# Kernel tuning notes

Measured on AMD Instinct MI355X. Metric: run time of the kernel, lower is better.

## Reference

```python
import jax, jax.numpy as jnp
import numpy as np

N, E = 50000, 800000
IN_C, H_C, OUT_C, HEADS = 64, 32, 32, 8


def setup_inputs() -> dict:
    key = jax.random.key(0)
    ks = jax.random.split(key, 16)
    def glorot(k, shape):
        fan_in = shape[-1]
        return jax.random.normal(k, shape, dtype=jnp.float32) / jnp.sqrt(jnp.float32(fan_in))
    inp = {
        'x': jax.random.normal(ks[0], (N, IN_C), dtype=jnp.float32),
        'edge_index': jax.random.randint(ks[1], (2, E), 0, N, dtype=jnp.int64),
        # layer 1: in_c -> h_c, heads
        'W1l': glorot(ks[2], (HEADS * H_C, IN_C)),
        'b1l': jnp.zeros((HEADS * H_C,), jnp.float32),
        'W1r': glorot(ks[3], (HEADS * H_C, IN_C)),
        'b1r': jnp.zeros((HEADS * H_C,), jnp.float32),
        'att1': glorot(ks[4], (HEADS, H_C)),
        'bias1': jnp.zeros((H_C,), jnp.float32),
        # layer 2: h_c -> out_c, heads
        'W2l': glorot(ks[5], (HEADS * OUT_C, H_C)),
        'b2l': jnp.zeros((HEADS * OUT_C,), jnp.float32),
        'W2r': glorot(ks[6], (HEADS * OUT_C, H_C)),
        'b2r': jnp.zeros((HEADS * OUT_C,), jnp.float32),
        'att2': glorot(ks[7], (HEADS, OUT_C)),
        'bias2': jnp.zeros((OUT_C,), jnp.float32),
    }
    return inp


def _gatv2_layer(x, src, dst, valid, Wl, bl, Wr, br, att, bias):
    # PyG GATv2Conv (share_weights=False, concat=False): message j->i uses
    # e = att . leaky_relu(lin_l(x_j) + lin_r(x_i), 0.2); softmax over dst; agg lin_l(x_j).
    n = x.shape[0]
    heads, c = att.shape
    xl = (x @ Wl.T + bl).reshape(n, heads, c)
    xr = (x @ Wr.T + br).reshape(n, heads, c)
    m = jax.nn.leaky_relu(xl[src] + xr[dst], negative_slope=0.2)  # [Etot,H,C]
    score = jnp.einsum('ehc,hc->eh', m, att)                      # [Etot,H]
    score = jnp.where(valid[:, None], score, -jnp.inf)
    smax = jax.ops.segment_max(score, dst, num_segments=n)        # [N,H]
    a = jnp.where(valid[:, None], jnp.exp(score - smax[dst]), 0.0)
    denom = jax.ops.segment_sum(a, dst, num_segments=n)
    a = a / jnp.maximum(denom[dst], 1e-16)
    out = jax.ops.segment_sum(a[..., None] * xl[src], dst, num_segments=n)  # [N,H,C]
    return out.mean(axis=1) + bias


def reference(x, edge_index, W1l, b1l, W1r, b1r, att1, bias1,
              W2l, b2l, W2r, b2r, att2, bias2):
    n = x.shape[0]
    src0, dst0 = edge_index[0], edge_index[1]
    # PyG removes existing self loops then adds fresh ones: mask originals,
    # append one self loop per node (keeps static shapes).
    loop = jnp.arange(n, dtype=src0.dtype)
    src = jnp.concatenate([src0, loop])
    dst = jnp.concatenate([dst0, loop])
    valid = jnp.concatenate([src0 != dst0, jnp.ones((n,), bool)])
    h = _gatv2_layer(x, src, dst, valid, W1l, b1l, W1r, b1r, att1, bias1)
    h = jax.nn.leaky_relu(h, negative_slope=0.01)  # nn.LeakyReLU default
    out = _gatv2_layer(h, src, dst, valid, W2l, b2l, W2r, b2r, att2, bias2)
    return out
```

## Files before the change

### kernel.cpp

```cpp
#include <hip/hip_runtime.h>
#include <math.h>

#define HEADS 8
#define CDIM 32
#define ODIM 256

typedef _Float16 h2 __attribute__((ext_vector_type(2)));
typedef _Float16 h4 __attribute__((ext_vector_type(4)));
typedef _Float16 h8 __attribute__((ext_vector_type(8)));
typedef float f32x4 __attribute__((ext_vector_type(4)));
union H4 { h4 v; h2 p[2]; };

#if __has_builtin(__builtin_amdgcn_fdot2)
#define FDOT2(a,b,c) __builtin_amdgcn_fdot2((a),(b),(c),false)
#else
static __device__ __forceinline__ float fdot2_sw(h2 a, h2 b, float c){
  return fmaf((float)a.x, (float)b.x, fmaf((float)a.y, (float)b.y, c));
}
#define FDOT2(a,b,c) fdot2_sw((a),(b),(c))
#endif

__device__ __forceinline__ float lrelu(float v, float s){ return fmaxf(v, s*v); }

__global__ void block_sum_kernel(const int* __restrict__ counts, int* __restrict__ bsums, int n){
  int i = blockIdx.x*256 + threadIdx.x;
  int v = (i < n) ? counts[i] : 0;
#pragma unroll
  for (int off=1; off<64; off<<=1) v += __shfl_xor(v, off);
  __shared__ int ws[4];
  int lane = threadIdx.x & 63, w = threadIdx.x >> 6;
  if (lane == 0) ws[w] = v;
  __syncthreads();
  if (threadIdx.x == 0) bsums[blockIdx.x] = ws[0]+ws[1]+ws[2]+ws[3];
}

__global__ __launch_bounds__(1024) void scan_bsums_kernel(int* __restrict__ bsums, int nb){
  __shared__ int s[1024];
  int t = threadIdx.x;
  int v = (t < nb) ? bsums[t] : 0;
  s[t] = v;
  __syncthreads();
  for (int off=1; off<1024; off<<=1){
    int u = (t >= off) ? s[t-off] : 0;
    __syncthreads();
    s[t] += u;
    __syncthreads();
  }
  if (t < nb) bsums[t] = s[t] - v;
}

__global__ void local_scan_kernel(const int* __restrict__ counts, const int* __restrict__ bsums,
                                  int* __restrict__ indptr, int n){
  __shared__ int s[256];
  int t = threadIdx.x;
  int i = blockIdx.x*256 + t;
  int v = (i < n) ? counts[i] : 0;
  s[t] = v;
  __syncthreads();
  for (int off=1; off<256; off<<=1){
    int u = (t >= off) ? s[t-off] : 0;
    __syncthreads();
    s[t] += u;
    __syncthreads();
  }
  int excl = s[t] - v + bsums[blockIdx.x];
  if (i < n) indptr[i] = excl;
  if (i == n-1) indptr[n] = excl + v;
}

__global__ void scatter_kernel(const int* __restrict__ src, const int* __restrict__ dst,
                               const int* __restrict__ rank, const int* __restrict__ indptr,
                               int* __restrict__ csr_src, int e){
  int i = blockIdx.x*256 + threadIdx.x;
  if (i < e){
    int r = rank[i];
    if (r >= 0){
      int d = dst[i];
      csr_src[indptr[d] + r] = src[i];
    }
  }
}

template<int K, bool FUSE_COUNT>
__global__ __launch_bounds__(256, 2) void gemm_mfma(const float* __restrict__ X,
    const float* __restrict__ Wl, const float* __restrict__ bl,
    const float* __restrict__ Wr, const float* __restrict__ br,
    _Float16* __restrict__ outl, _Float16* __restrict__ outr, int n,
    const int* __restrict__ src, const int* __restrict__ dst,
    int* __restrict__ counts, int* __restrict__ rank, int e){
  if (FUSE_COUNT && blockIdx.y == 0){
    int stride = gridDim.x*256;
    for (int i = blockIdx.x*256 + threadIdx.x; i < e; i += stride){
      int s = src[i], d = dst[i];
      int r = -1;
      if (s != d) r = atomicAdd(counts + d, 1);
      rank[i] = r;
    }
    return;
  }
  const int KP = K + 8;
  __shared__ __align__(16) _Float16 Xs[64*(K+8)];
  int t = threadIdx.x;
  int n0 = blockIdx.x*64;
  int ybase = FUSE_COUNT ? (blockIdx.y-1) : blockIdx.y;

  for (int idx = t; idx < 64*(K/4); idx += 256){
    int row = idx/(K/4), c = (idx%(K/4))*4;
    int node = n0 + row; if (node >= n) node = n-1;
    float4 xv = *(const float4*)(X + (size_t)node*K + c);
    h4 hv = {(_Float16)xv.x, (_Float16)xv.y, (_Float16)xv.z, (_Float16)xv.w};
    *(h4*)(Xs + row*KP + c) = hv;
  }
  __syncthreads();

  int wave = t >> 6, lane = t & 63;
  int co = ybase*256 + wave*64;
  const float* W   = (co < 256) ? Wl : Wr;
  const float* Bv  = (co < 256) ? bl : br;
  _Float16* outp   = (co < 256) ? outl : outr;
  int lco = co & 255;
  int lr = lane & 15, lg = lane >> 4;

  f32x4 acc[4][4];
#pragma unroll
  for (int c = 0; c < 4; ++c)
#pragma unroll
    for (int m = 0; m < 4; ++m) acc[c][m] = (f32x4){0.f, 0.f, 0.f, 0.f};

#pragma unroll
  for (int ks = 0; ks < K/32; ++ks){
    int k0 = ks*32 + lg*8;
    h8 a[4], b[4];
#pragma unroll
    for (int c = 0; c < 4; ++c){
      const float* wp = W + (size_t)(lco + c*16 + lr)*K + k0;
      float4 w0 = *(const float4*)(wp);
      float4 w1 = *(const float4*)(wp + 4);
      a[c] = (h8){(_Float16)w0.x,(_Float16)w0.y,(_Float16)w0.z,(_Float16)w0.w,
                  (_Float16)w1.x,(_Float16)w1.y,(_Float16)w1.z,(_Float16)w1.w};
    }
#pragma unroll
    for (int m = 0; m < 4; ++m)
      b[m] = *(const h8*)(Xs + (m*16 + lr)*KP + k0);
#pragma unroll
    for (int c = 0; c < 4; ++c)
#pragma unroll
      for (int m = 0; m < 4; ++m)
        acc[c][m] = __builtin_amdgcn_mfma_f32_16x16x32_f16(a[c], b[m], acc[c][m], 0, 0, 0);
  }

#pragma unroll
  for (int c = 0; c < 4; ++c){
    int ch = lco + c*16 + lg*4;
    float4 bb = *(const float4*)(Bv + ch);
#pragma unroll
    for (int m = 0; m < 4; ++m){
      int node = n0 + m*16 + lr;
      if (node < n){
        h4 o = {(_Float16)(acc[c][m][0] + bb.x), (_Float16)(acc[c][m][1] + bb.y),
                (_Float16)(acc[c][m][2] + bb.z), (_Float16)(acc[c][m][3] + bb.w)};
        *(h4*)(outp + (size_t)node*ODIM + ch) = o;
      }
    }
  }
}

__global__ __launch_bounds__(256) void edge_kernel(
    const _Float16* __restrict__ xl, const _Float16* __restrict__ xr,
    const float* __restrict__ att, const float* __restrict__ bias,
    const int* __restrict__ indptr, const int* __restrict__ csr_src,
    float* __restrict__ out, int n, int act)
{
  int wid = blockIdx.x*4 + (threadIdx.x >> 6);
  if (wid >= n) return;
  int lane = threadIdx.x & 63;
  const float LOG2E = 1.44269504088896341f;

  float4 attf = *(const float4*)(att + 4*lane);
  h2 at0 = (h2){(_Float16)(attf.x*LOG2E), (_Float16)(attf.y*LOG2E)};
  h2 at1 = (h2){(_Float16)(attf.z*LOG2E), (_Float16)(attf.w*LOG2E)};
  const h2 c02 = {(_Float16)0.2f, (_Float16)0.2f};

  H4 xrh; xrh.v = *(const h4*)(xr + (size_t)wid*ODIM + 4*lane);
  H4 self; self.v = *(const h4*)(xl + (size_t)wid*ODIM + 4*lane);

  auto score = [&](const H4& c)->float{
    h2 t0 = c.p[0] + xrh.p[0];
    h2 t1 = c.p[1] + xrh.p[1];
    h2 q0 = __builtin_elementwise_max(t0, t0 * c02);
    h2 q1 = __builtin_elementwise_max(t1, t1 * c02);
    float d = FDOT2(q0, at0, FDOT2(q1, at1, 0.f));
    d += __shfl_xor(d, 1);
    d += __shfl_xor(d, 2);
    d += __shfl_xor(d, 4);
    return d;
  };

  float w0 = exp2f(score(self));
  float denom = w0;
  float4 acc;
  acc.x = w0 * (float)self.v.x;
  acc.y = w0 * (float)self.v.y;
  acc.z = w0 * (float)self.v.z;
  acc.w = w0 * (float)self.v.w;

  int beg = __builtin_amdgcn_readfirstlane(indptr[wid]);
  int end = __builtin_amdgcn_readfirstlane(indptr[wid+1]);
  int cnt = end - beg;
  H4 r0, r1;
  r0.v = (h4){}; r1.v = (h4){};
  if (cnt > 0){
    int s0 = __builtin_amdgcn_readfirstlane(csr_src[beg]);
    r0.v = *(const h4*)(xl + (size_t)s0*ODIM + 4*lane);
  }
  if (cnt > 1){
    int s1 = __builtin_amdgcn_readfirstlane(csr_src[beg+1]);
    r1.v = *(const h4*)(xl + (size_t)s1*ODIM + 4*lane);
  }
  for (int k = 0; k < cnt; ++k){
    H4 cur = r0; r0 = r1;
    if (k+2 < cnt){
      int s2 = __builtin_amdgcn_readfirstlane(csr_src[beg+k+2]);
      r1.v = *(const h4*)(xl + (size_t)s2*ODIM + 4*lane);
    }
    float pe = exp2f(score(cur));
    denom += pe;
    acc.x = fmaf(pe, (float)cur.v.x, acc.x);
    acc.y = fmaf(pe, (float)cur.v.y, acc.y);
    acc.z = fmaf(pe, (float)cur.v.z, acc.z);
    acc.w = fmaf(pe, (float)cur.v.w, acc.w);
  }
  float inv = 1.f/denom;
  float vx = acc.x*inv, vy = acc.y*inv, vz = acc.z*inv, vw = acc.w*inv;
  vx += __shfl_xor(vx, 8);  vx += __shfl_xor(vx, 16);  vx += __shfl_xor(vx, 32);
  vy += __shfl_xor(vy, 8);  vy += __shfl_xor(vy, 16);  vy += __shfl_xor(vy, 32);
  vz += __shfl_xor(vz, 8);  vz += __shfl_xor(vz, 16);  vz += __shfl_xor(vz, 32);
  vw += __shfl_xor(vw, 8);  vw += __shfl_xor(vw, 16);  vw += __shfl_xor(vw, 32);
  if (lane < 8){
    float4 bv = *(const float4*)(bias + 4*lane);
    float ox = vx*0.125f + bv.x;
    float oy = vy*0.125f + bv.y;
    float oz = vz*0.125f + bv.z;
    float ow = vw*0.125f + bv.w;
    if (act){
      ox = lrelu(ox, 0.01f); oy = lrelu(oy, 0.01f);
      oz = lrelu(oz, 0.01f); ow = lrelu(ow, 0.01f);
    }
    *(float4*)(out + (size_t)wid*CDIM + 4*lane) = make_float4(ox, oy, oz, ow);
  }
}

extern "C" void kernel_launch(void* const* d_in, const int* in_sizes, int n_in,
                              void* d_out, int out_size, void* d_ws, size_t ws_size,
                              hipStream_t stream){
  (void)n_in; (void)out_size; (void)ws_size;
  const float* x    = (const float*)d_in[0];
  const int*   ei   = (const int*)d_in[1];
  const float* W1l  = (const float*)d_in[2];
  const float* b1l  = (const float*)d_in[3];
  const float* W1r  = (const float*)d_in[4];
  const float* b1r  = (const float*)d_in[5];
  const float* att1 = (const float*)d_in[6];
  const float* bias1= (const float*)d_in[7];
  const float* W2l  = (const float*)d_in[8];
  const float* b2l  = (const float*)d_in[9];
  const float* W2r  = (const float*)d_in[10];
  const float* b2r  = (const float*)d_in[11];
  const float* att2 = (const float*)d_in[12];
  const float* bias2= (const float*)d_in[13];
  int n = in_sizes[0] / 64;
  int e = in_sizes[1] / 2;
  const int* src = ei;
  const int* dst = ei + e;

  char* ws = (char*)d_ws;
  size_t off = 0;
  auto alloc = [&](size_t bytes)->char*{
    char* p = ws + off; off += (bytes + 255) & ~(size_t)255; return p;
  };
  _Float16* xl  = (_Float16*)alloc((size_t)n*ODIM*2);
  _Float16* xr  = (_Float16*)alloc((size_t)n*ODIM*2);
  float* h      = (float*)alloc((size_t)n*CDIM*4);
  int*   counts = (int*)alloc((size_t)n*4);
  int*   indptr = (int*)alloc((size_t)(n+1)*4);
  int*   rank   = (int*)alloc((size_t)e*4);
  int*   csr    = (int*)alloc((size_t)e*4);
  int*   bsums  = (int*)alloc((size_t)1024*4);

  int nblk = (n + 255) / 256;
  int nt64 = (n + 63) / 64;
  hipMemsetAsync(counts, 0, (size_t)n*4, stream);

  gemm_mfma<64,true><<<dim3(nt64,3), 256, 0, stream>>>(
      x, W1l, b1l, W1r, b1r, xl, xr, n, src, dst, counts, rank, e);
  block_sum_kernel<<<nblk, 256, 0, stream>>>(counts, bsums, n);
  scan_bsums_kernel<<<1, 1024, 0, stream>>>(bsums, nblk);
  local_scan_kernel<<<nblk, 256, 0, stream>>>(counts, bsums, indptr, n);
  scatter_kernel<<<(e+255)/256, 256, 0, stream>>>(src, dst, rank, indptr, csr, e);

  edge_kernel<<<(n+3)/4, 256, 0, stream>>>(xl, xr, att1, bias1, indptr, csr, h, n, 1);
  gemm_mfma<32,false><<<dim3(nt64,2), 256, 0, stream>>>(
      h, W2l, b2l, W2r, b2r, xl, xr, n, nullptr, nullptr, nullptr, nullptr, 0);
  edge_kernel<<<(n+3)/4, 256, 0, stream>>>(xl, xr, att2, bias2, indptr, csr, (float*)d_out, n, 0);
}
```

Before: 337.1 us.

## Replace global-atomic CSR build with two-level bucketed counting sort

Builds the destination-sorted CSR with a two-pass counting sort. Edges are first bucketed by dst>>7 using shared-memory histograms per 2048-edge chunk, then each bucket is sorted locally in shared memory. This replaces the global per-node atomic counting, the multi-kernel scan and the random scatter, aiming to cut global atomic contention and improve write locality. The edge counting is no longer fused into the first GEMM launch. The change adds more kernel launches, an extra packed edge buffer, and a source index packed into bits above position 7, which assumes source indices stay below 2^24.

```diff
diff --git a/kernel.cpp b/kernel.cpp
--- a/kernel.cpp
+++ b/kernel.cpp
@@ -4,6 +4,8 @@
 #define HEADS 8
 #define CDIM 32
 #define ODIM 256
+#define BKT_SHIFT 7
+#define CHUNK 2048
 
 typedef _Float16 h2 __attribute__((ext_vector_type(2)));
 typedef _Float16 h4 __attribute__((ext_vector_type(4)));
@@ -22,62 +24,114 @@
 
 __device__ __forceinline__ float lrelu(float v, float s){ return fmaxf(v, s*v); }
 
-__global__ void block_sum_kernel(const int* __restrict__ counts, int* __restrict__ bsums, int n){
-  int i = blockIdx.x*256 + threadIdx.x;
-  int v = (i < n) ? counts[i] : 0;
-#pragma unroll
-  for (int off=1; off<64; off<<=1) v += __shfl_xor(v, off);
-  __shared__ int ws[4];
-  int lane = threadIdx.x & 63, w = threadIdx.x >> 6;
-  if (lane == 0) ws[w] = v;
-  __syncthreads();
-  if (threadIdx.x == 0) bsums[blockIdx.x] = ws[0]+ws[1]+ws[2]+ws[3];
-}
-
-__global__ __launch_bounds__(1024) void scan_bsums_kernel(int* __restrict__ bsums, int nb){
-  __shared__ int s[1024];
+
+__global__ __launch_bounds__(256) void csr_hist_kernel(
+    const int* __restrict__ src, const int* __restrict__ dst,
+    int* __restrict__ rank, int* __restrict__ hist, int e, int B){
+  __shared__ int lh[512];
+  int t = threadIdx.x, k = blockIdx.x;
+  for (int b = t; b < B; b += 256) lh[b] = 0;
+  __syncthreads();
+  int base_i = k*CHUNK;
+#pragma unroll
+  for (int j = 0; j < CHUNK/256; ++j){
+    int i = base_i + j*256 + t;
+    if (i < e){
+      int s = src[i], d = dst[i];
+      int r = -1;
+      if (s != d) r = atomicAdd(&lh[d>>BKT_SHIFT], 1);
+      rank[i] = r;
+    }
+  }
+  __syncthreads();
+  for (int b = t; b < B; b += 256) hist[k*B + b] = lh[b];
+}
+
+__global__ __launch_bounds__(512) void csr_offs_kernel(
+    int* __restrict__ hist, int* __restrict__ btotal, int NB, int B){
+  __shared__ int s[512];
+  int b = blockIdx.x, t = threadIdx.x;
+  int v = (t < NB) ? hist[t*B + b] : 0;
+  s[t] = v;
+  __syncthreads();
+  for (int off=1; off<512; off<<=1){
+    int u = (t >= off) ? s[t-off] : 0;
+    __syncthreads(); s[t] += u; __syncthreads();
+  }
+  int excl = s[t] - v;
+  if (t < NB) hist[t*B + b] = excl;
+  if (t == NB-1) btotal[b] = excl + v;
+}
+
+__global__ __launch_bounds__(512) void csr_base_kernel(
+    const int* __restrict__ btotal, int* __restrict__ base, int B){
+  __shared__ int s[512];
   int t = threadIdx.x;
-  int v = (t < nb) ? bsums[t] : 0;
+  int v = (t < B) ? btotal[t] : 0;
   s[t] = v;
   __syncthreads();
-  for (int off=1; off<1024; off<<=1){
+  for (int off=1; off<512; off<<=1){
     int u = (t >= off) ? s[t-off] : 0;
+    __syncthreads(); s[t] += u; __syncthreads();
+  }
+  if (t < B) base[t] = s[t] - v;
+  if (t == B-1) base[B] = s[t];
+}
+
+__global__ __launch_bounds__(256) void csr_scatter_kernel(
+    const int* __restrict__ src, const int* __restrict__ dst,
+    const int* __restrict__ rank, const int* __restrict__ offs,
+    const int* __restrict__ base, int* __restrict__ bpack, int e, int B){
+  int t = threadIdx.x, k = blockIdx.x;
+  int base_i = k*CHUNK;
+#pragma unroll
+  for (int j = 0; j < CHUNK/256; ++j){
+    int i = base_i + j*256 + t;
+    if (i < e){
+      int r = rank[i];
+      if (r >= 0){
+        int d = dst[i], s = src[i];
+        int b = d >> BKT_SHIFT;
+        int pos = base[b] + offs[k*B + b] + r;
+        bpack[pos] = (s << BKT_SHIFT) | (d & 127);
+      }
+    }
+  }
+}
+
+__global__ __launch_bounds__(256) void csr_sort_kernel(
+    const int* __restrict__ bpack, const int* __restrict__ base,
+    int* __restrict__ csr, int* __restrict__ indptr, int n, int B){
+  __shared__ int lh[128], cur[128], ss[128];
+  int b = blockIdx.x, t = threadIdx.x;
+  int beg = base[b], cnt = base[b+1] - beg;
+  if (t < 128) lh[t] = 0;
+  __syncthreads();
+  for (int j = t; j < cnt; j += 256){
+    int p = bpack[beg + j];
+    atomicAdd(&lh[p & 127], 1);
+  }
+  __syncthreads();
+  int v = (t < 128) ? lh[t] : 0;
+  if (t < 128) ss[t] = v;
+  __syncthreads();
+  for (int off=1; off<128; off<<=1){
+    int u = (t >= off && t < 128) ? ss[t-off] : 0;
     __syncthreads();
-    s[t] += u;
+    if (t < 128) ss[t] += u;
     __syncthreads();
   }
-  if (t < nb) bsums[t] = s[t] - v;
-}
-
-__global__ void local_scan_kernel(const int* __restrict__ counts, const int* __restrict__ bsums,
-                                  int* __restrict__ indptr, int n){
-  __shared__ int s[256];
-  int t = threadIdx.x;
-  int i = blockIdx.x*256 + t;
-  int v = (i < n) ? counts[i] : 0;
-  s[t] = v;
-  __syncthreads();
-  for (int off=1; off<256; off<<=1){
-    int u = (t >= off) ? s[t-off] : 0;
-    __syncthreads();
-    s[t] += u;
-    __syncthreads();
-  }
-  int excl = s[t] - v + bsums[blockIdx.x];
-  if (i < n) indptr[i] = excl;
-  if (i == n-1) indptr[n] = excl + v;
-}
-
-__global__ void scatter_kernel(const int* __restrict__ src, const int* __restrict__ dst,
-                               const int* __restrict__ rank, const int* __restrict__ indptr,
-                               int* __restrict__ csr_src, int e){
-  int i = blockIdx.x*256 + threadIdx.x;
-  if (i < e){
-    int r = rank[i];
-    if (r >= 0){
-      int d = dst[i];
-      csr_src[indptr[d] + r] = src[i];
-    }
+  if (t < 128){
+    int excl = ss[t] - v;
+    cur[t] = excl;
+    int node = (b << BKT_SHIFT) + t;
+    if (node <= n) indptr[node] = beg + excl;
+  }
+  __syncthreads();
+  for (int j = t; j < cnt; j += 256){
+    int p = bpack[beg + j];
+    int lpos = atomicAdd(&cur[p & 127], 1);
+    csr[beg + lpos] = p >> BKT_SHIFT;
   }
 }
 
@@ -85,24 +139,12 @@
 __global__ __launch_bounds__(256, 2) void gemm_mfma(const float* __restrict__ X,
     const float* __restrict__ Wl, const float* __restrict__ bl,
     const float* __restrict__ Wr, const float* __restrict__ br,
-    _Float16* __restrict__ outl, _Float16* __restrict__ outr, int n,
-    const int* __restrict__ src, const int* __restrict__ dst,
-    int* __restrict__ counts, int* __restrict__ rank, int e){
-  if (FUSE_COUNT && blockIdx.y == 0){
-    int stride = gridDim.x*256;
-    for (int i = blockIdx.x*256 + threadIdx.x; i < e; i += stride){
-      int s = src[i], d = dst[i];
-      int r = -1;
-      if (s != d) r = atomicAdd(counts + d, 1);
-      rank[i] = r;
-    }
-    return;
-  }
+    _Float16* __restrict__ outl, _Float16* __restrict__ outr, int n){
   const int KP = K + 8;
   __shared__ __align__(16) _Float16 Xs[64*(K+8)];
   int t = threadIdx.x;
   int n0 = blockIdx.x*64;
-  int ybase = FUSE_COUNT ? (blockIdx.y-1) : blockIdx.y;
+  int ybase = blockIdx.y;
 
   for (int idx = t; idx < 64*(K/4); idx += 256){
     int row = idx/(K/4), c = (idx%(K/4))*4;
@@ -281,25 +323,29 @@
   _Float16* xl  = (_Float16*)alloc((size_t)n*ODIM*2);
   _Float16* xr  = (_Float16*)alloc((size_t)n*ODIM*2);
   float* h      = (float*)alloc((size_t)n*CDIM*4);
-  int*   counts = (int*)alloc((size_t)n*4);
   int*   indptr = (int*)alloc((size_t)(n+1)*4);
   int*   rank   = (int*)alloc((size_t)e*4);
   int*   csr    = (int*)alloc((size_t)e*4);
-  int*   bsums  = (int*)alloc((size_t)1024*4);
-
-  int nblk = (n + 255) / 256;
+  int*   bpack  = (int*)alloc((size_t)e*4);
+
+  int NB = (e + CHUNK-1) / CHUNK;
+  int B  = (n + 127) >> 7;
+  int*   hist   = (int*)alloc((size_t)NB*B*4);
+  int*   btotal = (int*)alloc((size_t)B*4);
+  int*   base   = (int*)alloc((size_t)(B+1)*4);
+
   int nt64 = (n + 63) / 64;
-  hipMemsetAsync(counts, 0, (size_t)n*4, stream);
-
-  gemm_mfma<64,true><<<dim3(nt64,3), 256, 0, stream>>>(
-      x, W1l, b1l, W1r, b1r, xl, xr, n, src, dst, counts, rank, e);
-  block_sum_kernel<<<nblk, 256, 0, stream>>>(counts, bsums, n);
-  scan_bsums_kernel<<<1, 1024, 0, stream>>>(bsums, nblk);
-  local_scan_kernel<<<nblk, 256, 0, stream>>>(counts, bsums, indptr, n);
-  scatter_kernel<<<(e+255)/256, 256, 0, stream>>>(src, dst, rank, indptr, csr, e);
-
+
+  csr_hist_kernel<<<NB, 256, 0, stream>>>(src, dst, rank, hist, e, B);
+  csr_offs_kernel<<<B, 512, 0, stream>>>(hist, btotal, NB, B);
+  csr_base_kernel<<<1, 512, 0, stream>>>(btotal, base, B);
+  csr_scatter_kernel<<<NB, 256, 0, stream>>>(src, dst, rank, hist, base, bpack, e, B);
+  csr_sort_kernel<<<B, 256, 0, stream>>>(bpack, base, csr, indptr, n, B);
+
+  gemm_mfma<64,false><<<dim3(nt64,2), 256, 0, stream>>>(
+      x, W1l, b1l, W1r, b1r, xl, xr, n);
   edge_kernel<<<(n+3)/4, 256, 0, stream>>>(xl, xr, att1, bias1, indptr, csr, h, n, 1);
   gemm_mfma<32,false><<<dim3(nt64,2), 256, 0, stream>>>(
-      h, W2l, b2l, W2r, b2r, xl, xr, n, nullptr, nullptr, nullptr, nullptr, 0);
+      h, W2l, b2l, W2r, b2r, xl, xr, n);
   edge_kernel<<<(n+3)/4, 256, 0, stream>>>(xl, xr, att2, bias2, indptr, csr, (float*)d_out, n, 0);
 }
```

Measured after the change: 320.0 us. 5.1% less time.
